# Performance work log

Hardware: AMD Instinct MI355X
Metric: run time of the kernel (lower is better)

The kernel has to match this reference:

```python
import jax, jax.numpy as jnp
import numpy as np

N_CHANNELS = 22
N_PATCHES = 64
N_NODES = N_CHANNELS * N_PATCHES  # 1408
EMBED_DIM = 256
N_HEADS = 4
HEAD_DIM = EMBED_DIM // N_HEADS
ALPHA = 0.15
TOP_P = 0.85
DIST_THRESH = 0.55
BATCH = 16

TCP_PAIRS = [('FP1','F7'),('F7','T3'),('T3','T5'),('T5','O1'),('FP2','F8'),('F8','T4'),('T4','T6'),('T6','O2'),('FP1','F3'),('F3','C3'),('C3','P3'),('P3','O1'),('FP2','F4'),('F4','C4'),('C4','P4'),('P4','O2'),('A1','T3'),('T3','C3'),('C3','CZ'),('CZ','C4'),('C4','T4'),('T4','A2')]
_ELECTRODE_3D = {'FP1':(-0.31,0.95,0.0),'FP2':(0.31,0.95,0.0),'F7':(-0.81,0.59,0.0),'F3':(-0.55,0.67,0.5),'FZ':(0.0,0.71,0.71),'F4':(0.55,0.67,0.5),'F8':(0.81,0.59,0.0),'T3':(-1.0,0.0,0.0),'C3':(-0.57,0.0,0.82),'CZ':(0.0,0.0,1.0),'C4':(0.57,0.0,0.82),'T4':(1.0,0.0,0.0),'T5':(-0.81,-0.59,0.0),'P3':(-0.55,-0.67,0.5),'PZ':(0.0,-0.71,0.71),'P4':(0.55,-0.67,0.5),'T6':(0.81,-0.59,0.0),'O1':(-0.31,-0.95,0.0),'O2':(0.31,-0.95,0.0),'A1':(-1.05,0.0,-0.3),'A2':(1.05,0.0,-0.3)}


def _build_masks():
    # channel positions = midpoint of each bipolar TCP pair -> [22,3]
    ch_pos = np.array([(np.array(_ELECTRODE_3D[a]) + np.array(_ELECTRODE_3D[b])) / 2.0 for a, b in TCP_PAIRS])
    d = np.linalg.norm(ch_pos[:, None, :] - ch_pos[None, :, :], axis=-1)
    ch_adj = (d < DIST_THRESH).astype(np.float32)
    np.fill_diagonal(ch_adj, 0.0)
    # node = ch * n_patches + t ; spatial edges only between same t: kron(ch_adj, I_P)
    spatial = np.kron(ch_adj, np.eye(N_PATCHES, dtype=np.float32))
    # temporal: same channel, |p - p'| == 1
    T = np.zeros((N_PATCHES, N_PATCHES), dtype=np.float32)
    idx = np.arange(N_PATCHES - 1)
    T[idx, idx + 1] = 1.0
    T[idx + 1, idx] = 1.0
    temporal = np.kron(np.eye(N_CHANNELS, dtype=np.float32), T)
    return jnp.asarray(temporal), jnp.asarray(spatial)


def setup_inputs() -> dict:
    key = jax.random.key(0)
    ks = jax.random.split(key, 8)
    D, H, HD = EMBED_DIM, N_HEADS, HEAD_DIM
    s = 1.0 / np.sqrt(D)
    x = jax.random.normal(ks[0], (BATCH, N_NODES, D), dtype=jnp.float32)
    proj_w = jax.random.uniform(ks[1], (H, HD, D), jnp.float32, -s, s)
    gate_w = jax.random.uniform(ks[2], (3, D), jnp.float32, -s, s)
    gate_b = jax.random.uniform(ks[3], (3,), jnp.float32, -s, s)
    score_w1 = jax.random.uniform(ks[4], (D // 2, D), jnp.float32, -s, s)
    score_b1 = jax.random.uniform(ks[5], (D // 2,), jnp.float32, -s, s)
    s2 = 1.0 / np.sqrt(D // 2)
    score_w2 = jax.random.uniform(ks[6], (1, D // 2), jnp.float32, -s2, s2)
    score_b2 = jax.random.uniform(ks[7], (1,), jnp.float32, -s2, s2)
    threshold = jnp.asarray(0.5, dtype=jnp.float32)
    temporal_mask, spatial_mask = _build_masks()
    return {"x": x, "proj_w": proj_w, "gate_w": gate_w, "gate_b": gate_b,
            "score_w1": score_w1, "score_b1": score_b1, "score_w2": score_w2,
            "score_b2": score_b2, "threshold": threshold,
            "temporal_mask": temporal_mask, "spatial_mask": spatial_mask}


def _safe_dist(d2):
    d2 = jnp.maximum(d2, 0.0)
    return jnp.where(d2 > 0, jnp.sqrt(jnp.where(d2 > 0, d2, 1.0)), 0.0)


def reference(x, proj_w, gate_w, gate_b, score_w1, score_b1, score_w2, score_b2,
              threshold, temporal_mask, spatial_mask):
    B, N, D = x.shape
    H = proj_w.shape[0]
    k = max(1, int(N * ALPHA))
    b_idx = jnp.arange(B)[:, None, None]
    r_idx = jnp.arange(N)[None, :, None]

    # ---- MultiHeadDistanceKNN: mean over heads of (knn-mask * gaussian sim) ----
    adj = jnp.zeros((B, N, N), x.dtype)
    for h in range(H):
        z = x @ proj_w[h].T                                  # [B,N,hd]
        sq = jnp.sum(z * z, axis=-1)                         # [B,N]
        d2 = sq[:, :, None] + sq[:, None, :] - 2.0 * jnp.einsum('bnd,bmd->bnm', z, z)
        dist = _safe_dist(d2)                                # [B,N,N]
        _, topk_idx = jax.lax.top_k(-dist, k)                # k smallest dists
        m = jnp.zeros((B, N, N), x.dtype).at[b_idx, r_idx, topk_idx].set(1.0)
        m = jnp.maximum(m, jnp.swapaxes(m, -1, -2))          # symmetrize
        sim = jnp.exp(-dist * dist / (2.0 * jnp.mean(dist) ** 2 + 1e-8))
        adj = adj + sim * m
    adj = adj / H

    # ---- Temporal / Spatial filters (fixed masks) ----
    adj_t = adj * temporal_mask[None]
    adj_s = adj * spatial_mask[None]

    # ---- Pathological filter: MLP node score -> outer product -> soft gate ----
    h1 = jax.nn.gelu(x @ score_w1.T + score_b1, approximate=False)
    scores = jax.nn.sigmoid((h1 @ score_w2.T + score_b2)[..., 0])    # [B,N]
    edge_w = scores[:, :, None] * scores[:, None, :]
    adj_p = adj * jax.nn.sigmoid((edge_w - threshold) * 10.0)

    # ---- NoisyGatedRouter (eval: no noise): softmax -> top-p truncate -> renorm ----
    probs = jax.nn.softmax(x @ gate_w.T + gate_b, axis=-1)           # [B,N,3]
    order = jnp.argsort(-probs, axis=-1)
    sp = jnp.take_along_axis(probs, order, axis=-1)
    keep = (jnp.cumsum(sp, axis=-1) - sp) < TOP_P
    sp = sp * keep.astype(sp.dtype)
    inv = jnp.argsort(order, axis=-1)
    w = jnp.take_along_axis(sp, inv, axis=-1)                        # scatter back
    w = w / (jnp.sum(w, axis=-1, keepdims=True) + 1e-8)              # [B,N,3]

    # ---- Mix filters with per-edge weights (w_i + w_j)/2 ----
    out = jnp.zeros_like(adj)
    for f, a in enumerate((adj_t, adj_s, adj_p)):
        wf = w[:, :, f]
        ewf = (wf[:, :, None] + wf[:, None, :]) * 0.5
        out = out + a * ewf
    return out
```

## Files before the change

### kernel.cpp

```cpp
#include <hip/hip_runtime.h>
#include <math.h>

typedef __attribute__((ext_vector_type(8))) short bf16x8;
typedef __attribute__((ext_vector_type(4))) float f32x4;

__device__ __forceinline__ float wsum64(float v) {
#pragma unroll
  for (int d = 32; d > 0; d >>= 1) v += __shfl_xor(v, d, 64);
  return v;
}

__device__ __forceinline__ unsigned short f2bf(float f) {
  unsigned u = __float_as_uint(f);
  u = (u + 0x7FFFu + ((u >> 16) & 1u)) >> 16;
  return (unsigned short)u;
}

__global__ void k_init(const float* __restrict__ smask, float* __restrict__ chadj,
                       double* __restrict__ sums) {
  int t = threadIdx.x;
  if (t < 4) sums[t] = 0.0;
  if (t < 484) {
    int c1 = t / 22, c2 = t % 22;
    chadj[t] = smask[(size_t)(c1 * 64) * 1408 + (size_t)c2 * 64];
  }
}

__global__ __launch_bounds__(256) void k_gemm_in(
    const float* __restrict__ x, const float* __restrict__ projw,
    const float* __restrict__ w1, float* __restrict__ z, float* __restrict__ zT,
    unsigned short* __restrict__ zb, float* __restrict__ h1) {
  __shared__ float xs[16][68];
  __shared__ float wsT[16][68];
  __shared__ float ldsT[64][65];
  int n0 = blockIdx.x * 64;
  int o0 = blockIdx.y * 64;
  int tid = threadIdx.x;
  int tx = tid & 15, ty = tid >> 4;
  float acc[4][4];
#pragma unroll
  for (int i = 0; i < 4; i++)
#pragma unroll
    for (int j = 0; j < 4; j++) acc[i][j] = 0.f;
  for (int kc = 0; kc < 16; kc++) {
#pragma unroll
    for (int rep = 0; rep < 4; rep++) {
      int e = tid + rep * 256;
      int n = e >> 4, k = e & 15;
      xs[k][n] = x[(size_t)(n0 + n) * 256 + kc * 16 + k];
      int row = o0 + n;
      wsT[k][n] = (row < 256) ? projw[(size_t)row * 256 + kc * 16 + k]
                              : w1[(size_t)(row - 256) * 256 + kc * 16 + k];
    }
    __syncthreads();
#pragma unroll
    for (int k = 0; k < 16; k++) {
      float4 a4 = *(const float4*)&xs[k][4 * ty];
      float4 w4 = *(const float4*)&wsT[k][4 * tx];
      float ar[4] = {a4.x, a4.y, a4.z, a4.w};
      float wr[4] = {w4.x, w4.y, w4.z, w4.w};
#pragma unroll
      for (int i = 0; i < 4; i++)
#pragma unroll
        for (int j = 0; j < 4; j++) acc[i][j] = fmaf(ar[i], wr[j], acc[i][j]);
    }
    __syncthreads();
  }
  if (blockIdx.y >= 4) {
#pragma unroll
    for (int i = 0; i < 4; i++) {
      size_t base = (size_t)(n0 + 4 * ty + i) * 128 + (o0 - 256) + 4 * tx;
      float4 t;
      t.x = acc[i][0]; t.y = acc[i][1]; t.z = acc[i][2]; t.w = acc[i][3];
      *(float4*)&h1[base] = t;
    }
  } else {
#pragma unroll
    for (int i = 0; i < 4; i++) {
      size_t base = (size_t)(n0 + 4 * ty + i) * 256 + o0 + 4 * tx;
      float4 t;
      t.x = acc[i][0]; t.y = acc[i][1]; t.z = acc[i][2]; t.w = acc[i][3];
      *(float4*)&z[base] = t;
      unsigned lo = (unsigned)f2bf(acc[i][0]) | ((unsigned)f2bf(acc[i][1]) << 16);
      unsigned hi = (unsigned)f2bf(acc[i][2]) | ((unsigned)f2bf(acc[i][3]) << 16);
      uint2 u2; u2.x = lo; u2.y = hi;
      *(uint2*)(zb + base) = u2;
    }
    __syncthreads();
#pragma unroll
    for (int i = 0; i < 4; i++)
#pragma unroll
      for (int j = 0; j < 4; j++) ldsT[4 * tx + j][4 * ty + i] = acc[i][j];
    __syncthreads();
    int bblk = blockIdx.x / 22;
    int nbase = (blockIdx.x % 22) * 64;
#pragma unroll
    for (int rep = 0; rep < 16; rep++) {
      int e = tid + rep * 256;
      int oo = e >> 6, nn = e & 63;
      zT[(size_t)((bblk * 4 + blockIdx.y) * 64 + oo) * 1408 + nbase + nn] = ldsT[oo][nn];
    }
  }
}

__global__ __launch_bounds__(256) void k_node(
    const float* __restrict__ x, const float* __restrict__ z,
    const float* __restrict__ h1, const float* __restrict__ gw,
    const float* __restrict__ gb, const float* __restrict__ b1,
    const float* __restrict__ w2, const float* __restrict__ b2v,
    float* __restrict__ sq, float4* __restrict__ wnode) {
  int tid = threadIdx.x;
  int w = tid >> 6, lane = tid & 63;
  int node = blockIdx.x * 4 + w;
  int b = node / 1408, n = node % 1408;
  const float* zr = z + (size_t)node * 256;
  const float* xr = x + (size_t)node * 256;
#pragma unroll
  for (int c = 0; c < 4; c++) {
    float val = zr[c * 64 + lane];
    float s = wsum64(val * val);
    if (lane == 0) sq[(size_t)(b * 4 + c) * 1408 + n] = s;
  }
  float gl[3];
#pragma unroll
  for (int f = 0; f < 3; f++) {
    float p = 0.f;
#pragma unroll
    for (int c = 0; c < 4; c++)
      p = fmaf(xr[c * 64 + lane], gw[f * 256 + c * 64 + lane], p);
    gl[f] = wsum64(p) + gb[f];
  }
  const float* hr = h1 + (size_t)node * 128;
  float ps = 0.f;
#pragma unroll
  for (int c = 0; c < 2; c++) {
    float t = hr[c * 64 + lane] + b1[c * 64 + lane];
    float g = 0.5f * t * (1.f + erff(t * 0.7071067811865475f));
    ps = fmaf(g, w2[c * 64 + lane], ps);
  }
  float sc = wsum64(ps) + b2v[0];
  sc = 1.f / (1.f + expf(-sc));
  float mx = fmaxf(gl[0], fmaxf(gl[1], gl[2]));
  float ex[3];
  float esum = 0.f;
#pragma unroll
  for (int f = 0; f < 3; f++) { ex[f] = expf(gl[f] - mx); esum += ex[f]; }
  float p3[3];
#pragma unroll
  for (int f = 0; f < 3; f++) p3[f] = ex[f] / esum;
  int rk[3];
#pragma unroll
  for (int f = 0; f < 3; f++) {
    int r = 0;
#pragma unroll
    for (int g = 0; g < 3; g++)
      r += ((p3[g] > p3[f]) || (p3[g] == p3[f] && g < f)) ? 1 : 0;
    rk[f] = r;
  }
  float sp[3]; int oi[3];
#pragma unroll
  for (int f = 0; f < 3; f++) { sp[rk[f]] = p3[f]; oi[rk[f]] = f; }
  bool k1 = sp[0] < 0.85f;
  bool k2 = (sp[0] + sp[1]) < 0.85f;
  float wv[3];
  wv[oi[0]] = sp[0];
  wv[oi[1]] = k1 ? sp[1] : 0.f;
  wv[oi[2]] = k2 ? sp[2] : 0.f;
  float inv = 1.f / (wv[0] + wv[1] + wv[2] + 1e-8f);
  if (lane == 0) wnode[node] = make_float4(wv[0] * inv, wv[1] * inv, wv[2] * inv, sc);
}

template <int TC>
__device__ __forceinline__ void dotstrip16(float (&v)[16][6],
                                           const float* __restrict__ zTh,
                                           int i0, int jb) {
#pragma unroll
  for (int r = 0; r < 16; r++)
#pragma unroll
    for (int t = 0; t < TC; t++) v[r][t] = 0.f;
  const float* ap = zTh + i0;
  const float* bp = zTh + jb;
  float bc[TC], ac[16];
#pragma unroll
  for (int t = 0; t < TC; t++) bc[t] = bp[t * 64];
#pragma unroll
  for (int r = 0; r < 16; r++) ac[r] = ap[r];
#pragma unroll 1
  for (int k = 0; k < 63; k++) {
    const float* bpn = bp + 1408;
    const float* apn = ap + 1408;
    float bn[TC], an[16];
#pragma unroll
    for (int t = 0; t < TC; t++) bn[t] = bpn[t * 64];
#pragma unroll
    for (int r = 0; r < 16; r++) an[r] = apn[r];
#pragma unroll
    for (int r = 0; r < 16; r++)
#pragma unroll
      for (int t = 0; t < TC; t++) v[r][t] = fmaf(ac[r], bc[t], v[r][t]);
    bp = bpn; ap = apn;
#pragma unroll
    for (int t = 0; t < TC; t++) bc[t] = bn[t];
#pragma unroll
    for (int r = 0; r < 16; r++) ac[r] = an[r];
  }
#pragma unroll
  for (int r = 0; r < 16; r++)
#pragma unroll
    for (int t = 0; t < TC; t++) v[r][t] = fmaf(ac[r], bc[t], v[r][t]);
}

__global__ __launch_bounds__(256, 2) void k_pass1(
    const float* __restrict__ zT, const float* __restrict__ sq,
    unsigned* __restrict__ bm, double* __restrict__ sums) {
  __shared__ unsigned hist[8][528];
  __shared__ float cand[16][128];
  __shared__ unsigned candCnt[16];
  __shared__ int tbinS[16], rstarS[16];
  __shared__ float TS[16];
  int b = blockIdx.y, h = blockIdx.z;
  int i0 = blockIdx.x * 16;
  int tid = threadIdx.x;
  int w = tid >> 6, lane = tid & 63;
  const float* zTh = zT + (size_t)((b * 4 + h) * 64) * 1408;
  const float* sqh = sq + (size_t)(b * 4 + h) * 1408;
  {
    unsigned* histF = &hist[0][0];
    for (int u = tid; u < 8 * 528; u += 256) histF[u] = 0u;
  }
  if (tid < 16) candCnt[tid] = 0u;
  __syncthreads();

  const int TC = (w < 2) ? 6 : 5;
  const int tbase = (w < 2) ? 6 * w : 5 * w + 2;
  int jb = tbase * 64 + lane;
  float sqj[6];
#pragma unroll
  for (int t = 0; t < 6; t++)
    sqj[t] = (t < 5 || TC == 6) ? sqh[jb + t * 64] : 0.f;

  float v[16][6];
  if (w < 2) dotstrip16<6>(v, zTh, i0, jb);
  else       dotstrip16<5>(v, zTh, i0, jb);

  float ssum = 0.f;
#pragma unroll
  for (int r = 0; r < 16; r++) {
    float sr = sqh[i0 + r];
#pragma unroll
    for (int t = 0; t < 6; t++) {
      if (t < 5 || TC == 6) {
        float d = sr + sqj[t] - 2.f * v[r][t];
        d = fmaxf(d, 0.f);
        ssum += sqrtf(d);
        v[r][t] = d;
        unsigned key = (unsigned)fminf(d * 4.0f, 511.0f);
        atomicAdd(&hist[r >> 1][key + (key >> 6)], 1u << ((r & 1) * 16));
      }
    }
  }
  __syncthreads();

#pragma unroll 1
  for (int q = 0; q < 4; q++) {
    int r = 4 * w + q;
    int sh = (r & 1) * 16;
    const unsigned* hrow = hist[r >> 1];
    unsigned partial = 0;
#pragma unroll
    for (int u = 0; u < 8; u++) {
      int bin = 8 * lane + u;
      partial += (hrow[bin + (bin >> 6)] >> sh) & 0xffffu;
    }
    unsigned inc = partial;
#pragma unroll
    for (int d = 1; d < 64; d <<= 1) {
      unsigned u2 = __shfl_up(inc, d, 64);
      if (lane >= d) inc += u2;
    }
    unsigned long long mk = __ballot(inc >= 211u);
    int Ls = __ffsll(mk) - 1;
    unsigned cbefore = (Ls > 0) ? (unsigned)__shfl((int)inc, Ls - 1, 64) : 0u;
    int tb = -1;
    unsigned run = cbefore, cbelow = cbefore;
#pragma unroll
    for (int u = 0; u < 8; u++) {
      int bin = 8 * Ls + u;
      unsigned c = (hrow[bin + (bin >> 6)] >> sh) & 0xffffu;
      if (tb < 0) {
        if (run + c >= 211u) { tb = bin; cbelow = run; }
        run += c;
      }
    }
    if (lane == 0) { tbinS[r] = tb; rstarS[r] = 211 - (int)cbelow; }
  }
  __syncthreads();

#pragma unroll
  for (int r = 0; r < 16; r++) {
    int tb = tbinS[r];
#pragma unroll
    for (int t = 0; t < 6; t++) {
      if (t < 5 || TC == 6) {
        float d = v[r][t];
        unsigned key = (unsigned)fminf(d * 4.0f, 511.0f);
        if ((int)key == tb) {
          unsigned id = atomicAdd(&candCnt[r], 1u);
          if (id < 128u) cand[r][id] = d;
        }
      }
    }
  }
  __syncthreads();

#pragma unroll 1
  for (int q = 0; q < 4; q++) {
    int r = 4 * w + q;
    int rstar = rstarS[r];
    unsigned craw = candCnt[r];
    int cnt = (craw > 128u) ? 128 : (int)craw;
    float t2l = INFINITY;
    for (int base = 0; base < cnt; base += 64) {
      int ci = base + lane;
      if (ci < cnt) {
        float xm = cand[r][ci];
        int below = 0, eq = 0;
        for (int m = 0; m < cnt; m++) {
          float y = cand[r][m];
          below += (y < xm) ? 1 : 0;
          eq += (y == xm) ? 1 : 0;
        }
        if (below < rstar && rstar <= below + eq) t2l = fminf(t2l, xm);
      }
    }
#pragma unroll
    for (int dd = 32; dd > 0; dd >>= 1) t2l = fminf(t2l, __shfl_xor(t2l, dd, 64));
    if (lane == 0) TS[r] = t2l;
  }
  __syncthreads();

#pragma unroll
  for (int r = 0; r < 16; r++) {
    float T = TS[r];
    unsigned* bmrow = bm + (size_t)((h * 16 + b) * 1408 + i0 + r) * 44;
#pragma unroll
    for (int t = 0; t < 6; t++) {
      if (t < 5 || TC == 6) {
        unsigned long long bl = __ballot(v[r][t] <= T);
        int tile = tbase + t;
        if (lane == 0) bmrow[tile * 2] = (unsigned)bl;
        if (lane == 32) bmrow[tile * 2 + 1] = (unsigned)(bl >> 32);
      }
    }
  }
  ssum = wsum64(ssum);
  if (lane == 0) atomicAdd(&sums[h], (double)ssum);
}

__global__ __launch_bounds__(256) void k_final(
    const unsigned short* __restrict__ zb, const float* __restrict__ sq,
    const float4* __restrict__ wnode, const unsigned* __restrict__ bm,
    const double* __restrict__ sums, const float* __restrict__ chadj,
    const float* __restrict__ thrp, float* __restrict__ out) {
  int it = blockIdx.x, jt = blockIdx.y, b = blockIdx.z;
  int tid = threadIdx.x, wv = tid >> 6, lane = tid & 63;
  int quad = lane >> 4, l15 = lane & 15;
  float c2h[4];
#pragma unroll
  for (int h = 0; h < 4; h++) {
    double mu = sums[h] * (1.0 / (16.0 * 1408.0 * 1408.0));
    c2h[h] = (float)(1.0 / (2.0 * mu * mu + 1e-8)) * 1.44269504088896f;
  }
  float thr = thrp[0];
  int ib = it * 64 + wv * 16;
  const unsigned short* za = zb + (size_t)(b * 1408 + ib + l15) * 256;
  bf16x8 af[4][2];
#pragma unroll
  for (int h = 0; h < 4; h++)
#pragma unroll
    for (int k0 = 0; k0 < 2; k0++)
      af[h][k0] = *(const bf16x8*)(za + h * 64 + k0 * 32 + quad * 8);
  int ibq = ib + quad * 4;
  float4 wi[4];
  float sqi[4][4];
#pragma unroll
  for (int reg = 0; reg < 4; reg++) {
    int i = ibq + reg;
    wi[reg] = wnode[b * 1408 + i];
#pragma unroll
    for (int h = 0; h < 4; h++) sqi[reg][h] = sq[(size_t)(b * 4 + h) * 1408 + i];
  }
#pragma unroll
  for (int js = 0; js < 4; js++) {
    int j = jt * 64 + js * 16 + l15;
    const unsigned short* zj = zb + (size_t)(b * 1408 + j) * 256;
    f32x4 acc[4];
#pragma unroll
    for (int h = 0; h < 4; h++) {
      bf16x8 b0 = *(const bf16x8*)(zj + h * 64 + quad * 8);
      bf16x8 b1f = *(const bf16x8*)(zj + h * 64 + 32 + quad * 8);
      f32x4 a = {0.f, 0.f, 0.f, 0.f};
      a = __builtin_amdgcn_mfma_f32_16x16x32_bf16(af[h][0], b0, a, 0, 0, 0);
      a = __builtin_amdgcn_mfma_f32_16x16x32_bf16(af[h][1], b1f, a, 0, 0, 0);
      acc[h] = a;
    }
    float sqj[4];
#pragma unroll
    for (int h = 0; h < 4; h++) sqj[h] = sq[(size_t)(b * 4 + h) * 1408 + j];
    float4 wj = wnode[b * 1408 + j];
    float adjv[4] = {0.f, 0.f, 0.f, 0.f};
#pragma unroll
    for (int h = 0; h < 4; h++) {
      const unsigned* bmh = bm + (size_t)(h * 16 + b) * 1408 * 44;
      unsigned wJ = bmh[(size_t)j * 44 + (ibq >> 5)];
#pragma unroll
      for (int reg = 0; reg < 4; reg++) {
        int i = ibq + reg;
        float d2 = sqi[reg][h] + sqj[h] - 2.f * acc[h][reg];
        d2 = fmaxf(d2, 0.f);
        float sim = exp2f(-d2 * c2h[h]);
        unsigned bi = bmh[(size_t)i * 44 + (j >> 5)] >> (j & 31);
        unsigned bj = wJ >> (i & 31);
        adjv[reg] += (((bi | bj) & 1u) != 0u) ? sim : 0.f;
      }
    }
#pragma unroll
    for (int reg = 0; reg < 4; reg++) {
      int i = ibq + reg;
      int chi = i >> 6, pi = i & 63, chj = j >> 6, pj = j & 63;
      float e0 = 0.5f * (wi[reg].x + wj.x);
      float e1 = 0.5f * (wi[reg].y + wj.y);
      float e2 = 0.5f * (wi[reg].z + wj.z);
      float a2 = 0.f;
      if (chi == chj) {
        int dp = pi - pj;
        if (dp == 1 || dp == -1) a2 += e0;
      }
      if (pi == pj && chadj[chi * 22 + chj] != 0.f) a2 += e1;
      float xw = (wi[reg].w * wj.w - thr) * 10.f;
      float pt = 1.f / (1.f + exp2f(-xw * 1.44269504088896f));
      a2 += pt * e2;
      out[(size_t)(b * 1408 + i) * 1408 + j] = 0.25f * adjv[reg] * a2;
    }
  }
}

extern "C" void kernel_launch(void* const* d_in, const int* in_sizes, int n_in,
                              void* d_out, int out_size, void* d_ws, size_t ws_size,
                              hipStream_t stream) {
  (void)in_sizes; (void)n_in; (void)out_size; (void)ws_size;
  const float* x = (const float*)d_in[0];
  const float* projw = (const float*)d_in[1];
  const float* gw = (const float*)d_in[2];
  const float* gb = (const float*)d_in[3];
  const float* w1 = (const float*)d_in[4];
  const float* b1 = (const float*)d_in[5];
  const float* w2 = (const float*)d_in[6];
  const float* b2 = (const float*)d_in[7];
  const float* thr = (const float*)d_in[8];
  const float* smask = (const float*)d_in[10];
  float* out = (float*)d_out;
  char* ws = (char*)d_ws;
  size_t off = 0;
  auto take = [&](size_t bytes) {
    char* p = ws + off;
    off += (bytes + 255) & ~(size_t)255;
    return p;
  };
  float* z = (float*)take((size_t)22528 * 256 * 4);
  float* zT = (float*)take((size_t)22528 * 256 * 4);
  unsigned short* zb = (unsigned short*)take((size_t)22528 * 256 * 2);
  float* h1 = (float*)take((size_t)22528 * 128 * 4);
  float* sq = (float*)take((size_t)16 * 4 * 1408 * 4);
  float4* wnode = (float4*)take((size_t)22528 * 16);
  unsigned* bm = (unsigned*)take((size_t)4 * 16 * 1408 * 44 * 4);
  float* chadj = (float*)take(484 * 4);
  double* sums = (double*)take(4 * 8);

  hipLaunchKernelGGL(k_init, dim3(1), dim3(512), 0, stream, smask, chadj, sums);
  hipLaunchKernelGGL(k_gemm_in, dim3(352, 6), dim3(256), 0, stream, x, projw, w1,
                     z, zT, zb, h1);
  hipLaunchKernelGGL(k_node, dim3(5632), dim3(256), 0, stream, x, z, h1, gw, gb,
                     b1, w2, b2, sq, wnode);
  hipLaunchKernelGGL(k_pass1, dim3(88, 16, 4), dim3(256), 0, stream, zT, sq, bm,
                     sums);
  hipLaunchKernelGGL(k_final, dim3(22, 22, 16), dim3(256), 0, stream, zb, sq,
                     wnode, bm, sums, chadj, thr, out);
}
```

Before: 1.109 ms.

## Compute pass1 pairwise distances with split-bf16 MFMA instead of FP32 FMA

Splits z into three bf16 components (hi, lo, lo2) and computes the per-head pairwise dot products in k_pass1 with 16x16x32 bf16 MFMA, using six cross products to emulate FP32 accuracy. The transposed zT buffer and its LDS transpose are dropped. Distances are recomputed in a second MFMA pass, so register-resident distance arrays are no longer needed. The bitmask is built in LDS from a below-bin ballot plus candidate indices. This trades extra matrix work for removing the scalar FMA bottleneck. It risks small precision differences at threshold ties.

```diff
diff --git a/kernel.cpp b/kernel.cpp
--- a/kernel.cpp
+++ b/kernel.cpp
@@ -14,6 +14,10 @@
   unsigned u = __float_as_uint(f);
   u = (u + 0x7FFFu + ((u >> 16) & 1u)) >> 16;
   return (unsigned short)u;
+}
+
+__device__ __forceinline__ float bf2f(unsigned short h) {
+  return __uint_as_float((unsigned)h << 16);
 }
 
 __global__ void k_init(const float* __restrict__ smask, float* __restrict__ chadj,
@@ -28,11 +32,11 @@
 
 __global__ __launch_bounds__(256) void k_gemm_in(
     const float* __restrict__ x, const float* __restrict__ projw,
-    const float* __restrict__ w1, float* __restrict__ z, float* __restrict__ zT,
-    unsigned short* __restrict__ zb, float* __restrict__ h1) {
+    const float* __restrict__ w1, float* __restrict__ z,
+    unsigned short* __restrict__ zb, unsigned short* __restrict__ zbl,
+    unsigned short* __restrict__ zbl2, float* __restrict__ h1) {
   __shared__ float xs[16][68];
   __shared__ float wsT[16][68];
-  __shared__ float ldsT[64][65];
   int n0 = blockIdx.x * 64;
   int o0 = blockIdx.y * 64;
   int tid = threadIdx.x;
@@ -81,24 +85,27 @@
       float4 t;
       t.x = acc[i][0]; t.y = acc[i][1]; t.z = acc[i][2]; t.w = acc[i][3];
       *(float4*)&z[base] = t;
-      unsigned lo = (unsigned)f2bf(acc[i][0]) | ((unsigned)f2bf(acc[i][1]) << 16);
-      unsigned hi = (unsigned)f2bf(acc[i][2]) | ((unsigned)f2bf(acc[i][3]) << 16);
-      uint2 u2; u2.x = lo; u2.y = hi;
+      unsigned short hh[4], ll[4], mm[4];
+#pragma unroll
+      for (int j = 0; j < 4; j++) {
+        float xv = acc[i][j];
+        unsigned short h0 = f2bf(xv);
+        float r1 = xv - bf2f(h0);
+        unsigned short h1v = f2bf(r1);
+        float r2 = r1 - bf2f(h1v);
+        unsigned short h2 = f2bf(r2);
+        hh[j] = h0; ll[j] = h1v; mm[j] = h2;
+      }
+      uint2 u2;
+      u2.x = (unsigned)hh[0] | ((unsigned)hh[1] << 16);
+      u2.y = (unsigned)hh[2] | ((unsigned)hh[3] << 16);
       *(uint2*)(zb + base) = u2;
-    }
-    __syncthreads();
-#pragma unroll
-    for (int i = 0; i < 4; i++)
-#pragma unroll
-      for (int j = 0; j < 4; j++) ldsT[4 * tx + j][4 * ty + i] = acc[i][j];
-    __syncthreads();
-    int bblk = blockIdx.x / 22;
-    int nbase = (blockIdx.x % 22) * 64;
-#pragma unroll
-    for (int rep = 0; rep < 16; rep++) {
-      int e = tid + rep * 256;
-      int oo = e >> 6, nn = e & 63;
-      zT[(size_t)((bblk * 4 + blockIdx.y) * 64 + oo) * 1408 + nbase + nn] = ldsT[oo][nn];
+      u2.x = (unsigned)ll[0] | ((unsigned)ll[1] << 16);
+      u2.y = (unsigned)ll[2] | ((unsigned)ll[3] << 16);
+      *(uint2*)(zbl + base) = u2;
+      u2.x = (unsigned)mm[0] | ((unsigned)mm[1] << 16);
+      u2.y = (unsigned)mm[2] | ((unsigned)mm[3] << 16);
+      *(uint2*)(zbl2 + base) = u2;
     }
   }
 }
@@ -170,93 +177,77 @@
   if (lane == 0) wnode[node] = make_float4(wv[0] * inv, wv[1] * inv, wv[2] * inv, sc);
 }
 
-template <int TC>
-__device__ __forceinline__ void dotstrip16(float (&v)[16][6],
-                                           const float* __restrict__ zTh,
-                                           int i0, int jb) {
-#pragma unroll
-  for (int r = 0; r < 16; r++)
-#pragma unroll
-    for (int t = 0; t < TC; t++) v[r][t] = 0.f;
-  const float* ap = zTh + i0;
-  const float* bp = zTh + jb;
-  float bc[TC], ac[16];
-#pragma unroll
-  for (int t = 0; t < TC; t++) bc[t] = bp[t * 64];
-#pragma unroll
-  for (int r = 0; r < 16; r++) ac[r] = ap[r];
-#pragma unroll 1
-  for (int k = 0; k < 63; k++) {
-    const float* bpn = bp + 1408;
-    const float* apn = ap + 1408;
-    float bn[TC], an[16];
-#pragma unroll
-    for (int t = 0; t < TC; t++) bn[t] = bpn[t * 64];
-#pragma unroll
-    for (int r = 0; r < 16; r++) an[r] = apn[r];
-#pragma unroll
-    for (int r = 0; r < 16; r++)
-#pragma unroll
-      for (int t = 0; t < TC; t++) v[r][t] = fmaf(ac[r], bc[t], v[r][t]);
-    bp = bpn; ap = apn;
-#pragma unroll
-    for (int t = 0; t < TC; t++) bc[t] = bn[t];
-#pragma unroll
-    for (int r = 0; r < 16; r++) ac[r] = an[r];
-  }
-#pragma unroll
-  for (int r = 0; r < 16; r++)
-#pragma unroll
-    for (int t = 0; t < TC; t++) v[r][t] = fmaf(ac[r], bc[t], v[r][t]);
-}
-
 __global__ __launch_bounds__(256, 2) void k_pass1(
-    const float* __restrict__ zT, const float* __restrict__ sq,
+    const unsigned short* __restrict__ zb, const unsigned short* __restrict__ zbl,
+    const unsigned short* __restrict__ zbl2, const float* __restrict__ sq,
     unsigned* __restrict__ bm, double* __restrict__ sums) {
   __shared__ unsigned hist[8][528];
-  __shared__ float cand[16][128];
+  __shared__ float candD[16][128];
+  __shared__ unsigned short candJ[16][128];
   __shared__ unsigned candCnt[16];
   __shared__ int tbinS[16], rstarS[16];
   __shared__ float TS[16];
+  __shared__ unsigned bmL[16][44];
+  __shared__ float srowL[16];
   int b = blockIdx.y, h = blockIdx.z;
   int i0 = blockIdx.x * 16;
-  int tid = threadIdx.x;
-  int w = tid >> 6, lane = tid & 63;
-  const float* zTh = zT + (size_t)((b * 4 + h) * 64) * 1408;
+  int tid = threadIdx.x, w = tid >> 6, lane = tid & 63;
+  int quad = lane >> 4, l15 = lane & 15;
   const float* sqh = sq + (size_t)(b * 4 + h) * 1408;
   {
-    unsigned* histF = &hist[0][0];
-    for (int u = tid; u < 8 * 528; u += 256) histF[u] = 0u;
-  }
-  if (tid < 16) candCnt[tid] = 0u;
-  __syncthreads();
-
-  const int TC = (w < 2) ? 6 : 5;
-  const int tbase = (w < 2) ? 6 * w : 5 * w + 2;
-  int jb = tbase * 64 + lane;
-  float sqj[6];
-#pragma unroll
-  for (int t = 0; t < 6; t++)
-    sqj[t] = (t < 5 || TC == 6) ? sqh[jb + t * 64] : 0.f;
-
-  float v[16][6];
-  if (w < 2) dotstrip16<6>(v, zTh, i0, jb);
-  else       dotstrip16<5>(v, zTh, i0, jb);
+    unsigned* hf = &hist[0][0];
+    for (int u = tid; u < 8 * 528; u += 256) hf[u] = 0u;
+  }
+  if (tid < 16) { candCnt[tid] = 0u; srowL[tid] = sqh[i0 + tid]; }
+  __syncthreads();
+
+  size_t abase = ((size_t)(b * 1408 + i0 + l15)) * 256 + h * 64;
+  bf16x8 ah[2], al[2], am[2];
+#pragma unroll
+  for (int k0 = 0; k0 < 2; k0++) {
+    ah[k0] = *(const bf16x8*)(zb + abase + k0 * 32 + quad * 8);
+    al[k0] = *(const bf16x8*)(zbl + abase + k0 * 32 + quad * 8);
+    am[k0] = *(const bf16x8*)(zbl2 + abase + k0 * 32 + quad * 8);
+  }
+
+  auto tdot = [&](int tile) -> f32x4 {
+    size_t jb = ((size_t)(b * 1408 + tile * 16 + l15)) * 256 + h * 64;
+    bf16x8 bh0 = *(const bf16x8*)(zb + jb + quad * 8);
+    bf16x8 bh1 = *(const bf16x8*)(zb + jb + 32 + quad * 8);
+    bf16x8 bl0 = *(const bf16x8*)(zbl + jb + quad * 8);
+    bf16x8 bl1 = *(const bf16x8*)(zbl + jb + 32 + quad * 8);
+    bf16x8 bm0 = *(const bf16x8*)(zbl2 + jb + quad * 8);
+    bf16x8 bm1 = *(const bf16x8*)(zbl2 + jb + 32 + quad * 8);
+    f32x4 a = {0.f, 0.f, 0.f, 0.f};
+    a = __builtin_amdgcn_mfma_f32_16x16x32_bf16(ah[0], bh0, a, 0, 0, 0);
+    a = __builtin_amdgcn_mfma_f32_16x16x32_bf16(ah[1], bh1, a, 0, 0, 0);
+    a = __builtin_amdgcn_mfma_f32_16x16x32_bf16(ah[0], bl0, a, 0, 0, 0);
+    a = __builtin_amdgcn_mfma_f32_16x16x32_bf16(ah[1], bl1, a, 0, 0, 0);
+    a = __builtin_amdgcn_mfma_f32_16x16x32_bf16(al[0], bh0, a, 0, 0, 0);
+    a = __builtin_amdgcn_mfma_f32_16x16x32_bf16(al[1], bh1, a, 0, 0, 0);
+    a = __builtin_amdgcn_mfma_f32_16x16x32_bf16(al[0], bl0, a, 0, 0, 0);
+    a = __builtin_amdgcn_mfma_f32_16x16x32_bf16(al[1], bl1, a, 0, 0, 0);
+    a = __builtin_amdgcn_mfma_f32_16x16x32_bf16(ah[0], bm0, a, 0, 0, 0);
+    a = __builtin_amdgcn_mfma_f32_16x16x32_bf16(ah[1], bm1, a, 0, 0, 0);
+    a = __builtin_amdgcn_mfma_f32_16x16x32_bf16(am[0], bh0, a, 0, 0, 0);
+    a = __builtin_amdgcn_mfma_f32_16x16x32_bf16(am[1], bh1, a, 0, 0, 0);
+    return a;
+  };
 
   float ssum = 0.f;
-#pragma unroll
-  for (int r = 0; r < 16; r++) {
-    float sr = sqh[i0 + r];
-#pragma unroll
-    for (int t = 0; t < 6; t++) {
-      if (t < 5 || TC == 6) {
-        float d = sr + sqj[t] - 2.f * v[r][t];
-        d = fmaxf(d, 0.f);
-        ssum += sqrtf(d);
-        v[r][t] = d;
-        unsigned key = (unsigned)fminf(d * 4.0f, 511.0f);
-        atomicAdd(&hist[r >> 1][key + (key >> 6)], 1u << ((r & 1) * 16));
-      }
+#pragma unroll 1
+  for (int t = 0; t < 22; t++) {
+    int tile = w * 22 + t;
+    f32x4 acc = tdot(tile);
+    float sqjv = sqh[tile * 16 + l15];
+#pragma unroll
+    for (int reg = 0; reg < 4; reg++) {
+      int row = quad * 4 + reg;
+      float d = srowL[row] + sqjv - 2.f * acc[reg];
+      d = fmaxf(d, 0.f);
+      ssum += sqrtf(d);
+      unsigned key = (unsigned)fminf(d * 4.0f, 511.0f);
+      atomicAdd(&hist[row >> 1][key + (key >> 6)], 1u << ((row & 1) * 16));
     }
   }
   __syncthreads();
@@ -296,17 +287,28 @@
   }
   __syncthreads();
 
-#pragma unroll
-  for (int r = 0; r < 16; r++) {
-    int tb = tbinS[r];
-#pragma unroll
-    for (int t = 0; t < 6; t++) {
-      if (t < 5 || TC == 6) {
-        float d = v[r][t];
-        unsigned key = (unsigned)fminf(d * 4.0f, 511.0f);
-        if ((int)key == tb) {
-          unsigned id = atomicAdd(&candCnt[r], 1u);
-          if (id < 128u) cand[r][id] = d;
+#pragma unroll 1
+  for (int t = 0; t < 22; t++) {
+    int tile = w * 22 + t;
+    f32x4 acc = tdot(tile);
+    float sqjv = sqh[tile * 16 + l15];
+#pragma unroll
+    for (int reg = 0; reg < 4; reg++) {
+      int row = quad * 4 + reg;
+      float d = srowL[row] + sqjv - 2.f * acc[reg];
+      d = fmaxf(d, 0.f);
+      unsigned key = (unsigned)fminf(d * 4.0f, 511.0f);
+      int tb = tbinS[row];
+      unsigned long long bl = __ballot((int)key < tb);
+      if (l15 == 0)
+        ((unsigned short*)&bmL[row & 3 ? row : row][0])[tile] = 0;
+      if (l15 == 0)
+        ((unsigned short*)&bmL[row][0])[tile] = (unsigned short)(bl >> (quad * 16));
+      if ((int)key == tb) {
+        unsigned id = atomicAdd(&candCnt[row], 1u);
+        if (id < 128u) {
+          candD[row][id] = d;
+          candJ[row][id] = (unsigned short)(tile * 16 + l15);
         }
       }
     }
@@ -323,10 +325,10 @@
     for (int base = 0; base < cnt; base += 64) {
       int ci = base + lane;
       if (ci < cnt) {
-        float xm = cand[r][ci];
+        float xm = candD[r][ci];
         int below = 0, eq = 0;
         for (int m = 0; m < cnt; m++) {
-          float y = cand[r][m];
+          float y = candD[r][m];
           below += (y < xm) ? 1 : 0;
           eq += (y == xm) ? 1 : 0;
         }
@@ -339,19 +341,24 @@
   }
   __syncthreads();
 
-#pragma unroll
-  for (int r = 0; r < 16; r++) {
-    float T = TS[r];
-    unsigned* bmrow = bm + (size_t)((h * 16 + b) * 1408 + i0 + r) * 44;
-#pragma unroll
-    for (int t = 0; t < 6; t++) {
-      if (t < 5 || TC == 6) {
-        unsigned long long bl = __ballot(v[r][t] <= T);
-        int tile = tbase + t;
-        if (lane == 0) bmrow[tile * 2] = (unsigned)bl;
-        if (lane == 32) bmrow[tile * 2 + 1] = (unsigned)(bl >> 32);
-      }
-    }
+#pragma unroll 1
+  for (int q = 0; q < 4; q++) {
+    int row = 4 * w + q;
+    float T = TS[row];
+    unsigned craw = candCnt[row];
+    int cnt = (craw > 128u) ? 128 : (int)craw;
+    for (int ci = lane; ci < cnt; ci += 64) {
+      if (candD[row][ci] <= T) {
+        int j = candJ[row][ci];
+        atomicOr(&bmL[row][j >> 5], 1u << (j & 31));
+      }
+    }
+  }
+  __syncthreads();
+
+  for (int u = tid; u < 16 * 44; u += 256) {
+    int row = u / 44, wd = u % 44;
+    bm[((size_t)((h * 16 + b) * 1408 + i0 + row)) * 44 + wd] = bmL[row][wd];
   }
   ssum = wsum64(ssum);
   if (lane == 0) atomicAdd(&sums[h], (double)ssum);
@@ -468,8 +475,9 @@
     return p;
   };
   float* z = (float*)take((size_t)22528 * 256 * 4);
-  float* zT = (float*)take((size_t)22528 * 256 * 4);
   unsigned short* zb = (unsigned short*)take((size_t)22528 * 256 * 2);
+  unsigned short* zbl = (unsigned short*)take((size_t)22528 * 256 * 2);
+  unsigned short* zbl2 = (unsigned short*)take((size_t)22528 * 256 * 2);
   float* h1 = (float*)take((size_t)22528 * 128 * 4);
   float* sq = (float*)take((size_t)16 * 4 * 1408 * 4);
   float4* wnode = (float4*)take((size_t)22528 * 16);
@@ -479,11 +487,11 @@
 
   hipLaunchKernelGGL(k_init, dim3(1), dim3(512), 0, stream, smask, chadj, sums);
   hipLaunchKernelGGL(k_gemm_in, dim3(352, 6), dim3(256), 0, stream, x, projw, w1,
-                     z, zT, zb, h1);
+                     z, zb, zbl, zbl2, h1);
   hipLaunchKernelGGL(k_node, dim3(5632), dim3(256), 0, stream, x, z, h1, gw, gb,
                      b1, w2, b2, sq, wnode);
-  hipLaunchKernelGGL(k_pass1, dim3(88, 16, 4), dim3(256), 0, stream, zT, sq, bm,
-                     sums);
+  hipLaunchKernelGGL(k_pass1, dim3(88, 16, 4), dim3(256), 0, stream, zb, zbl,
+                     zbl2, sq, bm, sums);
   hipLaunchKernelGGL(k_final, dim3(22, 22, 16), dim3(256), 0, stream, zb, sq,
                      wnode, bm, sums, chadj, thr, out);
 }
```

Result: slower. 1.246 ms (+12.3%).
